# Optimization experiments

Measured on AMD Instinct MI355X. Metric: run time of the kernel, lower is better.

The kernel has to match this reference:

```python
import jax, jax.numpy as jnp
import numpy as np
import math

B, S, HID = 4, 2048, 1024
NH, HD = 16, 64  # num heads, head dim
ROPE_THETA = 10000.0


def rotate_half(x):
    x1, x2 = jnp.split(x, 2, axis=-1)
    return jnp.concatenate((-x2, x1), axis=-1)


def setup_inputs() -> dict:
    key = jax.random.key(0)
    ks = jax.random.split(key, 7)
    hidden_states = jax.random.normal(ks[0], (B, S, HID), dtype=jnp.float32)
    attention_mask = jnp.zeros((B, 1, S, S), dtype=jnp.float32)
    position_ids = jnp.sort(jax.random.randint(ks[1], (B, S), 0, S), axis=-1)
    scale = 1.0 / math.sqrt(HID)
    Wq = jax.random.normal(ks[2], (HID, HID), dtype=jnp.float32) * scale
    Wk = jax.random.normal(ks[3], (HID, HID), dtype=jnp.float32) * scale
    Wv = jax.random.normal(ks[4], (HID, HID), dtype=jnp.float32) * scale
    Wo = jax.random.normal(ks[5], (HID, HID), dtype=jnp.float32) * scale
    return {"hidden_states": hidden_states, "attention_mask": attention_mask,
            "position_ids": position_ids, "Wq": Wq, "Wk": Wk, "Wv": Wv, "Wo": Wo}


def reference(hidden_states, attention_mask, position_ids, Wq, Wk, Wv, Wo):
    dtype = hidden_states.dtype
    # QKV projections (torch Linear: x @ W.T), reshape to [B, H, S, D]
    def proj(W):
        return (hidden_states @ W.T).reshape(B, S, NH, HD).transpose(0, 2, 1, 3)
    q, k, v = proj(Wq), proj(Wk), proj(Wv)

    # Rotary embeddings: cos/sin cache of shape [S, HD], gathered by position_ids
    inv_freq = 1.0 / (ROPE_THETA ** (jnp.arange(0, HD, 2, dtype=jnp.float32) / HD))
    t = jnp.arange(S, dtype=jnp.float32)
    freqs = t[:, None] * inv_freq[None, :]            # [S, HD/2]
    emb = jnp.concatenate((freqs, freqs), axis=-1)     # [S, HD]
    cos = jnp.cos(emb).astype(dtype)[position_ids][:, None]  # [B, 1, S, HD]
    sin = jnp.sin(emb).astype(dtype)[position_ids][:, None]

    q = q * cos + rotate_half(q) * sin
    k = k * cos + rotate_half(k) * sin

    # Manual attention: scores, additive mask, fp32 softmax, weighted sum
    scores = jnp.einsum('bhqd,bhkd->bhqk', q, k) / math.sqrt(HD)
    scores = scores + attention_mask
    attn = jax.nn.softmax(scores.astype(jnp.float32), axis=-1).astype(dtype)
    out = jnp.einsum('bhqk,bhkd->bhqd', attn, v)       # [B, H, S, D]
    out = out.transpose(0, 2, 1, 3).reshape(B, S, HID)
    return out @ Wo.T
```

## Files before the change

kernel.cpp:

```cpp
#include <hip/hip_runtime.h>
#include <hip/hip_bf16.h>
#include <math.h>

typedef __bf16 bf16;
typedef bf16 bf16x4 __attribute__((ext_vector_type(4)));
typedef bf16 bf16x8 __attribute__((ext_vector_type(8)));
typedef float f32x4 __attribute__((ext_vector_type(4)));

#define B_ 4
#define S_ 2048
#define HID_ 1024
#define NH_ 16
#define HD_ 64
#define LTS 72

__device__ __forceinline__ void async16(const bf16* g, bf16* l) {
  __builtin_amdgcn_global_load_lds(
      (const __attribute__((address_space(1))) void*)g,
      (__attribute__((address_space(3))) void*)l, 16, 0, 0);
}

#define MM16(A, B, C) C = __builtin_amdgcn_mfma_f32_16x16x32_bf16(A, B, C, 0, 0, 0)

__global__ void cvt_kernel(const float* __restrict__ src, bf16* __restrict__ dst, int n4) {
  int i = blockIdx.x * 256 + threadIdx.x;
  if (i < n4) {
    float4 v = ((const float4*)src)[i];
    bf16x4 o;
    o[0] = (bf16)v.x; o[1] = (bf16)v.y; o[2] = (bf16)v.z; o[3] = (bf16)v.w;
    ((bf16x4*)dst)[i] = o;
  }
}

#define DECL_ACC \
  f32x4 a00 = {}, a01 = {}, a02 = {}, a03 = {}; \
  f32x4 a10 = {}, a11 = {}, a12 = {}, a13 = {}; \
  f32x4 a20 = {}, a21 = {}, a22 = {}, a23 = {}; \
  f32x4 a30 = {}, a31 = {}, a32 = {}, a33 = {};

#define KLOOP_FRAGS_MFMA \
    bf16x8 af0 = *(const bf16x8*)(lA + (wm + 0 * 16 + l16) * 32 + quad * 8); \
    bf16x8 af1 = *(const bf16x8*)(lA + (wm + 1 * 16 + l16) * 32 + quad * 8); \
    bf16x8 af2 = *(const bf16x8*)(lA + (wm + 2 * 16 + l16) * 32 + quad * 8); \
    bf16x8 af3 = *(const bf16x8*)(lA + (wm + 3 * 16 + l16) * 32 + quad * 8); \
    bf16x8 bg0 = *(const bf16x8*)(lB + (wn + 0 * 16 + l16) * 32 + quad * 8); \
    bf16x8 bg1 = *(const bf16x8*)(lB + (wn + 1 * 16 + l16) * 32 + quad * 8); \
    bf16x8 bg2 = *(const bf16x8*)(lB + (wn + 2 * 16 + l16) * 32 + quad * 8); \
    bf16x8 bg3 = *(const bf16x8*)(lB + (wn + 3 * 16 + l16) * 32 + quad * 8); \
    MM16(af0, bg0, a00); MM16(af0, bg1, a01); MM16(af0, bg2, a02); MM16(af0, bg3, a03); \
    MM16(af1, bg0, a10); MM16(af1, bg1, a11); MM16(af1, bg2, a12); MM16(af1, bg3, a13); \
    MM16(af2, bg0, a20); MM16(af2, bg1, a21); MM16(af2, bg2, a22); MM16(af2, bg3, a23); \
    MM16(af3, bg0, a30); MM16(af3, bg1, a31); MM16(af3, bg2, a32); MM16(af3, bg3, a33);

#define ROPE_R(i, r, C0, C1, C2, C3) { \
  const int mloc = (i) * 16 + quad * 4 + (r); \
  const float p = (float)pos[mbase + mloc]; \
  const float aa0 = p * invf0, aa1 = p * invf1; \
  const float c0 = __cosf(aa0), sn0 = __sinf(aa0); \
  const float c1 = __cosf(aa1), sn1 = __sinf(aa1); \
  myT[mloc * LTS + l16]      = (bf16)((C0[r] * c0 - C2[r] * sn0) * scl); \
  myT[mloc * LTS + 32 + l16] = (bf16)((C2[r] * c0 + C0[r] * sn0) * scl); \
  myT[mloc * LTS + 16 + l16] = (bf16)((C1[r] * c1 - C3[r] * sn1) * scl); \
  myT[mloc * LTS + 48 + l16] = (bf16)((C3[r] * c1 + C1[r] * sn1) * scl); }
#define ROPE_I(i, C0, C1, C2, C3) \
  ROPE_R(i, 0, C0, C1, C2, C3) ROPE_R(i, 1, C0, C1, C2, C3) \
  ROPE_R(i, 2, C0, C1, C2, C3) ROPE_R(i, 3, C0, C1, C2, C3)

#define VW(i, j, C) { \
  bf16x4 o; o[0] = (bf16)C[0]; o[1] = (bf16)C[1]; o[2] = (bf16)C[2]; o[3] = (bf16)C[3]; \
  *(bf16x4*)(myT + ((j) * 16 + l16) * LTS + (i) * 16 + quad * 4) = o; }

__global__ void qkv_gemm(
    const bf16* __restrict__ X, const bf16* __restrict__ Wq,
    const bf16* __restrict__ Wk, const bf16* __restrict__ Wv,
    const int* __restrict__ pos,
    bf16* __restrict__ Q, bf16* __restrict__ Ko, bf16* __restrict__ Vt) {
  const int z = blockIdx.z;
  const bf16* W = (z == 0) ? Wq : (z == 1) ? Wk : Wv;
  const int m0 = blockIdx.y * 128;
  const int n0 = blockIdx.x * 128;
  __shared__ __align__(16) bf16 lA[128 * 32];
  __shared__ __align__(16) bf16 lB[128 * 32];
  __shared__ __align__(16) bf16 lT[4][64 * LTS];
  const int tid = threadIdx.x;
  const int lane = tid & 63, w = tid >> 6;
  const int wm = (w >> 1) * 64, wn = (w & 1) * 64;
  const int quad = lane >> 4, l16 = lane & 15;

  DECL_ACC

  const int qa = tid, qb = tid + 256;
  const int ra = qa >> 2, ca = (qa & 3) * 8;
  const int rb = qb >> 2, cb = (qb & 3) * 8;

  for (int k0 = 0; k0 < 1024; k0 += 32) {
    async16(X + (size_t)(m0 + ra) * 1024 + k0 + ca, lA + qa * 8);
    async16(X + (size_t)(m0 + rb) * 1024 + k0 + cb, lA + qb * 8);
    async16(W + (size_t)(n0 + ra) * 1024 + k0 + ca, lB + qa * 8);
    async16(W + (size_t)(n0 + rb) * 1024 + k0 + cb, lB + qb * 8);
    __syncthreads();
    KLOOP_FRAGS_MFMA
    __syncthreads();
  }

  const int h = (n0 + wn) >> 6;
  const int mbase = m0 + wm;
  const int b = mbase >> 11, s0 = mbase & 2047;
  bf16* myT = lT[w];

  if (z <= 1) {
    const float scl = (z == 0) ? 0.125f : 1.0f;
    const float invf0 = __expf(-0.28782313662425572f * (float)l16);
    const float invf1 = __expf(-0.28782313662425572f * (float)(16 + l16));
    ROPE_I(0, a00, a01, a02, a03)
    ROPE_I(1, a10, a11, a12, a13)
    ROPE_I(2, a20, a21, a22, a23)
    ROPE_I(3, a30, a31, a32, a33)
    asm volatile("s_waitcnt lgkmcnt(0)" ::: "memory");
    bf16* dst = (z == 0) ? Q : Ko;
    const int rr = lane >> 3, cc = lane & 7;
#pragma unroll
    for (int it = 0; it < 8; it++) {
      int mloc = it * 8 + rr;
      bf16x8 v = *(const bf16x8*)(myT + mloc * LTS + cc * 8);
      *(bf16x8*)(dst + (((size_t)b * NH_ + h) * S_ + s0 + mloc) * HD_ + cc * 8) = v;
    }
  } else {
    VW(0, 0, a00) VW(0, 1, a01) VW(0, 2, a02) VW(0, 3, a03)
    VW(1, 0, a10) VW(1, 1, a11) VW(1, 2, a12) VW(1, 3, a13)
    VW(2, 0, a20) VW(2, 1, a21) VW(2, 2, a22) VW(2, 3, a23)
    VW(3, 0, a30) VW(3, 1, a31) VW(3, 2, a32) VW(3, 3, a33)
    asm volatile("s_waitcnt lgkmcnt(0)" ::: "memory");
    const int rr = lane >> 3, cc = lane & 7;
#pragma unroll
    for (int it = 0; it < 8; it++) {
      int d = it * 8 + rr;
      bf16x8 v = *(const bf16x8*)(myT + d * LTS + cc * 8);
      *(bf16x8*)(Vt + (((size_t)b * NH_ + h) * HD_ + d) * S_ + s0 + cc * 8) = v;
    }
  }
}

__global__ void __launch_bounds__(256, 4) attn_kernel(
    const bf16* __restrict__ Q, const bf16* __restrict__ K,
    const bf16* __restrict__ Vt, const float* __restrict__ mask,
    bf16* __restrict__ ctx) {
  const int b = blockIdx.y >> 4, h = blockIdx.y & 15;
  const int q0 = blockIdx.x * 64;
  __shared__ __align__(16) bf16 lK[2][64 * 64];
  __shared__ __align__(16) bf16 lV[2][64 * 64];
  __shared__ __align__(16) bf16 lP[4][16 * 64];
  const int tid = threadIdx.x;
  const int lane = tid & 63, w = tid >> 6;
  const int quad = lane >> 4, l16 = lane & 15;

  const int sr = tid >> 3;
  const int scs = (tid & 7) ^ (sr & 7);

  const size_t headoff = ((size_t)b * NH_ + h) * S_ * HD_;
  {
    const bf16* src = Q + headoff + (size_t)q0 * HD_;
    async16(src + sr * 64 + scs * 8, lK[1] + tid * 8);
    async16(src + (sr + 32) * 64 + scs * 8, lK[1] + (tid + 256) * 8);
    const bf16* ksrc = K + headoff;
    async16(ksrc + sr * 64 + scs * 8, lK[0] + tid * 8);
    async16(ksrc + (sr + 32) * 64 + scs * 8, lK[0] + (tid + 256) * 8);
    const bf16* vbase = Vt + headoff;
    async16(vbase + (size_t)sr * S_ + scs * 8, lV[0] + tid * 8);
    async16(vbase + (size_t)(sr + 32) * S_ + scs * 8, lV[0] + (tid + 256) * 8);
  }

  const float* mrow = mask + ((size_t)b * S_ + q0 + w * 16 + l16) * S_;
  const int sw = l16 & 7;
  const int pq  = (quad ^ sw) * 8;
  const int pq2 = ((quad + 4) ^ sw) * 8;
  bf16* myP = lP[w];

  const float LOG2E = 1.44269504089f;
  const float MSH = -17.3123404907f;
#define XMASK(dst, src) { float4 t_ = (src); \
  dst.x = fmaf(t_.x, LOG2E, MSH); dst.y = fmaf(t_.y, LOG2E, MSH); \
  dst.z = fmaf(t_.z, LOG2E, MSH); dst.w = fmaf(t_.w, LOG2E, MSH); }

  float4 f0, f1, f2, f3;
  {
    const float4* m4 = (const float4*)(mrow);
    XMASK(f0, m4[quad]); XMASK(f1, m4[4 + quad]);
    XMASK(f2, m4[8 + quad]); XMASK(f3, m4[12 + quad]);
  }

  __syncthreads();
  const bf16x8 qf  = *(const bf16x8*)(lK[1] + (w * 16 + l16) * 64 + pq);
  const bf16x8 qf2 = *(const bf16x8*)(lK[1] + (w * 16 + l16) * 64 + pq2);
  __syncthreads();

  f32x4 o0 = {}, o1 = {}, o2 = {}, o3 = {};
  float l_acc = 0.f;

  for (int kt = 0; kt < 32; kt++) {
    const bf16* lKc = lK[kt & 1];
    const bf16* lVc = lV[kt & 1];
    if (kt < 31) {
      bf16* nK = lK[(kt & 1) ^ 1];
      bf16* nV = lV[(kt & 1) ^ 1];
      const int k0n = (kt + 1) * 64;
      const bf16* ksrc = K + headoff + (size_t)k0n * HD_;
      async16(ksrc + sr * 64 + scs * 8, nK + tid * 8);
      async16(ksrc + (sr + 32) * 64 + scs * 8, nK + (tid + 256) * 8);
      const bf16* vbase = Vt + headoff + k0n;
      async16(vbase + (size_t)sr * S_ + scs * 8, nV + tid * 8);
      async16(vbase + (size_t)(sr + 32) * S_ + scs * 8, nV + (tid + 256) * 8);
    }

    f32x4 s0 = {}, s1 = {}, s2 = {}, s3 = {};
    __builtin_amdgcn_s_setprio(1);
    {
      bf16x8 k0f = *(const bf16x8*)(lKc + (0 * 16 + l16) * 64 + pq);
      bf16x8 k1f = *(const bf16x8*)(lKc + (1 * 16 + l16) * 64 + pq);
      bf16x8 k2f = *(const bf16x8*)(lKc + (2 * 16 + l16) * 64 + pq);
      bf16x8 k3f = *(const bf16x8*)(lKc + (3 * 16 + l16) * 64 + pq);
      MM16(k0f, qf, s0); MM16(k1f, qf, s1); MM16(k2f, qf, s2); MM16(k3f, qf, s3);
    }
    {
      bf16x8 k0f = *(const bf16x8*)(lKc + (0 * 16 + l16) * 64 + pq2);
      bf16x8 k1f = *(const bf16x8*)(lKc + (1 * 16 + l16) * 64 + pq2);
      bf16x8 k2f = *(const bf16x8*)(lKc + (2 * 16 + l16) * 64 + pq2);
      bf16x8 k3f = *(const bf16x8*)(lKc + (3 * 16 + l16) * 64 + pq2);
      MM16(k0f, qf2, s0); MM16(k1f, qf2, s1); MM16(k2f, qf2, s2); MM16(k3f, qf2, s3);
    }
    __builtin_amdgcn_s_setprio(0);

    float p00 = __builtin_amdgcn_exp2f(fmaf(s0[0], LOG2E, f0.x));
    float p01 = __builtin_amdgcn_exp2f(fmaf(s0[1], LOG2E, f0.y));
    float p02 = __builtin_amdgcn_exp2f(fmaf(s0[2], LOG2E, f0.z));
    float p03 = __builtin_amdgcn_exp2f(fmaf(s0[3], LOG2E, f0.w));
    float p10 = __builtin_amdgcn_exp2f(fmaf(s1[0], LOG2E, f1.x));
    float p11 = __builtin_amdgcn_exp2f(fmaf(s1[1], LOG2E, f1.y));
    float p12 = __builtin_amdgcn_exp2f(fmaf(s1[2], LOG2E, f1.z));
    float p13 = __builtin_amdgcn_exp2f(fmaf(s1[3], LOG2E, f1.w));
    float p20 = __builtin_amdgcn_exp2f(fmaf(s2[0], LOG2E, f2.x));
    float p21 = __builtin_amdgcn_exp2f(fmaf(s2[1], LOG2E, f2.y));
    float p22 = __builtin_amdgcn_exp2f(fmaf(s2[2], LOG2E, f2.z));
    float p23 = __builtin_amdgcn_exp2f(fmaf(s2[3], LOG2E, f2.w));
    float p30 = __builtin_amdgcn_exp2f(fmaf(s3[0], LOG2E, f3.x));
    float p31 = __builtin_amdgcn_exp2f(fmaf(s3[1], LOG2E, f3.y));
    float p32 = __builtin_amdgcn_exp2f(fmaf(s3[2], LOG2E, f3.z));
    float p33 = __builtin_amdgcn_exp2f(fmaf(s3[3], LOG2E, f3.w));

    {
      const int swz = 8 * sw;
      bf16x4 pk;
      pk[0] = (bf16)p00; pk[1] = (bf16)p01; pk[2] = (bf16)p02; pk[3] = (bf16)p03;
      *(bf16x4*)(myP + l16 * 64 + ((0 * 16 + quad * 4) ^ swz)) = pk;
      pk[0] = (bf16)p10; pk[1] = (bf16)p11; pk[2] = (bf16)p12; pk[3] = (bf16)p13;
      *(bf16x4*)(myP + l16 * 64 + ((1 * 16 + quad * 4) ^ swz)) = pk;
      pk[0] = (bf16)p20; pk[1] = (bf16)p21; pk[2] = (bf16)p22; pk[3] = (bf16)p23;
      *(bf16x4*)(myP + l16 * 64 + ((2 * 16 + quad * 4) ^ swz)) = pk;
      pk[0] = (bf16)p30; pk[1] = (bf16)p31; pk[2] = (bf16)p32; pk[3] = (bf16)p33;
      *(bf16x4*)(myP + l16 * 64 + ((3 * 16 + quad * 4) ^ swz)) = pk;
    }

    l_acc += (((p00 + p01) + (p02 + p03)) + ((p10 + p11) + (p12 + p13)))
           + (((p20 + p21) + (p22 + p23)) + ((p30 + p31) + (p32 + p33)));

    if (kt < 31) {
      const float4* mn = (const float4*)(mrow + (kt + 1) * 64);
      XMASK(f0, mn[quad]); XMASK(f1, mn[4 + quad]);
      XMASK(f2, mn[8 + quad]); XMASK(f3, mn[12 + quad]);
    }

    __builtin_amdgcn_s_setprio(1);
    {
      bf16x8 ap = *(const bf16x8*)(myP + l16 * 64 + pq);
      bf16x8 b0 = *(const bf16x8*)(lVc + (0 * 16 + l16) * 64 + pq);
      bf16x8 b1 = *(const bf16x8*)(lVc + (1 * 16 + l16) * 64 + pq);
      bf16x8 b2 = *(const bf16x8*)(lVc + (2 * 16 + l16) * 64 + pq);
      bf16x8 b3 = *(const bf16x8*)(lVc + (3 * 16 + l16) * 64 + pq);
      MM16(ap, b0, o0); MM16(ap, b1, o1); MM16(ap, b2, o2); MM16(ap, b3, o3);
    }
    {
      bf16x8 ap = *(const bf16x8*)(myP + l16 * 64 + pq2);
      bf16x8 b0 = *(const bf16x8*)(lVc + (0 * 16 + l16) * 64 + pq2);
      bf16x8 b1 = *(const bf16x8*)(lVc + (1 * 16 + l16) * 64 + pq2);
      bf16x8 b2 = *(const bf16x8*)(lVc + (2 * 16 + l16) * 64 + pq2);
      bf16x8 b3 = *(const bf16x8*)(lVc + (3 * 16 + l16) * 64 + pq2);
      MM16(ap, b0, o0); MM16(ap, b1, o1); MM16(ap, b2, o2); MM16(ap, b3, o3);
    }
    __builtin_amdgcn_s_setprio(0);

    __syncthreads();
  }

  float l_run = l_acc;
  l_run += __shfl_xor(l_run, 16);
  l_run += __shfl_xor(l_run, 32);
  f32x4 lv;
  lv[0] = __shfl(l_run, quad * 4 + 0);
  lv[1] = __shfl(l_run, quad * 4 + 1);
  lv[2] = __shfl(l_run, quad * 4 + 2);
  lv[3] = __shfl(l_run, quad * 4 + 3);
  bf16* lO = lK[0];
#pragma unroll
  for (int r = 0; r < 4; r++) {
    const float invl = 1.0f / lv[r];
    const int sloc = w * 16 + quad * 4 + r;
    lO[sloc * 64 + l16]      = (bf16)(o0[r] * invl);
    lO[sloc * 64 + 16 + l16] = (bf16)(o1[r] * invl);
    lO[sloc * 64 + 32 + l16] = (bf16)(o2[r] * invl);
    lO[sloc * 64 + 48 + l16] = (bf16)(o3[r] * invl);
  }
  __syncthreads();
  {
    const int rr = tid >> 3, cc = tid & 7;
#pragma unroll
    for (int it = 0; it < 2; it++) {
      int sloc = it * 32 + rr;
      bf16x8 v = *(const bf16x8*)(lO + sloc * 64 + cc * 8);
      *(bf16x8*)(ctx + ((size_t)b * S_ + q0 + sloc) * HID_ + h * HD_ + cc * 8) = v;
    }
  }
}

#define PW(i, j, C) { \
  float* po = out + (size_t)(m0 + wm + (i) * 16 + quad * 4) * 1024 + n0 + wn + (j) * 16 + l16; \
  po[0] = C[0]; po[1024] = C[1]; po[2048] = C[2]; po[3072] = C[3]; }

__global__ void proj_gemm(
    const bf16* __restrict__ A, const bf16* __restrict__ Wo, float* __restrict__ out) {
  const int m0 = blockIdx.y * 128;
  const int n0 = blockIdx.x * 128;
  __shared__ __align__(16) bf16 lA[128 * 32];
  __shared__ __align__(16) bf16 lB[128 * 32];
  const int tid = threadIdx.x;
  const int lane = tid & 63, w = tid >> 6;
  const int wm = (w >> 1) * 64, wn = (w & 1) * 64;
  const int quad = lane >> 4, l16 = lane & 15;

  DECL_ACC
  const int qa = tid, qb = tid + 256;
  const int ra = qa >> 2, ca = (qa & 3) * 8;
  const int rb = qb >> 2, cb = (qb & 3) * 8;

  for (int k0 = 0; k0 < 1024; k0 += 32) {
    async16(A + (size_t)(m0 + ra) * 1024 + k0 + ca, lA + qa * 8);
    async16(A + (size_t)(m0 + rb) * 1024 + k0 + cb, lA + qb * 8);
    async16(Wo + (size_t)(n0 + ra) * 1024 + k0 + ca, lB + qa * 8);
    async16(Wo + (size_t)(n0 + rb) * 1024 + k0 + cb, lB + qb * 8);
    __syncthreads();
    KLOOP_FRAGS_MFMA
    __syncthreads();
  }
  PW(0, 0, a00) PW(0, 1, a01) PW(0, 2, a02) PW(0, 3, a03)
  PW(1, 0, a10) PW(1, 1, a11) PW(1, 2, a12) PW(1, 3, a13)
  PW(2, 0, a20) PW(2, 1, a21) PW(2, 2, a22) PW(2, 3, a23)
  PW(3, 0, a30) PW(3, 1, a31) PW(3, 2, a32) PW(3, 3, a33)
}

__global__ void sentinel_kernel(float* out, int n, float val) {
  int i = blockIdx.x * 256 + threadIdx.x;
  if (i < n) out[i] = val;
}

extern "C" void kernel_launch(void* const* d_in, const int* in_sizes, int n_in,
                              void* d_out, int out_size, void* d_ws, size_t ws_size,
                              hipStream_t stream) {
  const float* X    = (const float*)d_in[0];
  const float* mask = (const float*)d_in[1];
  const int*   pos  = (const int*)d_in[2];
  const float* Wq   = (const float*)d_in[3];
  const float* Wk   = (const float*)d_in[4];
  const float* Wv   = (const float*)d_in[5];
  const float* Wo   = (const float*)d_in[6];
  float* out = (float*)d_out;

  char* ws = (char*)d_ws;
  const size_t SZ = (size_t)B_ * NH_ * S_ * HD_ * sizeof(bf16);
  if (ws_size < 3 * SZ) {
    sentinel_kernel<<<(out_size + 255) / 256, 256, 0, stream>>>(
        out, out_size, (float)(ws_size >> 20));
    return;
  }

  bf16* Xb  = (bf16*)(ws);
  bf16* ctx = (bf16*)(ws);
  bf16* Q   = (bf16*)(ws + SZ);
  bf16* Vt  = (bf16*)(ws + 2 * SZ);
  bf16* Wob = (bf16*)(ws + 2 * SZ);
  bf16* Kb  = (bf16*)d_out;
  bf16* Wqb = (bf16*)((char*)d_out + SZ);
  bf16* Wkb = Wqb + 1024 * 1024;
  bf16* Wvb = Wkb + 1024 * 1024;

  const int nX4 = (B_ * S_ * HID_) / 4;
  const int nW4 = (HID_ * HID_) / 4;
  cvt_kernel<<<(nX4 + 255) / 256, 256, 0, stream>>>(X, Xb, nX4);
  cvt_kernel<<<(nW4 + 255) / 256, 256, 0, stream>>>(Wq, Wqb, nW4);
  cvt_kernel<<<(nW4 + 255) / 256, 256, 0, stream>>>(Wk, Wkb, nW4);
  cvt_kernel<<<(nW4 + 255) / 256, 256, 0, stream>>>(Wv, Wvb, nW4);

  qkv_gemm<<<dim3(8, 64, 3), 256, 0, stream>>>(Xb, Wqb, Wkb, Wvb, pos, Q, Kb, Vt);
  attn_kernel<<<dim3(32, 64), 256, 0, stream>>>(Q, Kb, Vt, mask, ctx);

  cvt_kernel<<<(nW4 + 255) / 256, 256, 0, stream>>>(Wo, Wob, nW4);
  proj_gemm<<<dim3(8, 64), 256, 0, stream>>>(ctx, Wob, out);
}
```

Baseline: 392.4 us.

## Process 128 query rows per attention block with 8 waves sharing K/V tiles

Doubles the attention block to 512 threads covering 128 query rows, so each K/V tile loaded into LDS is reused by twice as many waves and each thread issues one async load per tile instead of two. The P staging buffer is shrunk to 16x32 per wave, and P is written and read back in two halves just before each PV MFMA pair, using a new swizzle. Q is staged through spare LDS regions (lV[1] and lP), and the output epilogue reuses the whole lK area for 128 rows. The trade is fewer blocks in the grid and more waves per barrier, plus tighter LDS reuse that depends on the aliasing being correct.

```diff
diff --git a/kernel.cpp b/kernel.cpp
--- a/kernel.cpp
+++ b/kernel.cpp
@@ -141,15 +141,18 @@
   }
 }
 
-__global__ void __launch_bounds__(256, 4) attn_kernel(
+__global__ void __launch_bounds__(512, 4) attn_kernel(
     const bf16* __restrict__ Q, const bf16* __restrict__ K,
     const bf16* __restrict__ Vt, const float* __restrict__ mask,
     bf16* __restrict__ ctx) {
   const int b = blockIdx.y >> 4, h = blockIdx.y & 15;
-  const int q0 = blockIdx.x * 64;
+  const int q0 = blockIdx.x * 128;
   __shared__ __align__(16) bf16 lK[2][64 * 64];
   __shared__ __align__(16) bf16 lV[2][64 * 64];
-  __shared__ __align__(16) bf16 lP[4][16 * 64];
+  __shared__ __align__(16) bf16 lP[8][16 * 32];
+  bf16* lKf = (bf16*)lK;
+  bf16* lPf = (bf16*)lP;
+
   const int tid = threadIdx.x;
   const int lane = tid & 63, w = tid >> 6;
   const int quad = lane >> 4, l16 = lane & 15;
@@ -159,15 +162,11 @@
 
   const size_t headoff = ((size_t)b * NH_ + h) * S_ * HD_;
   {
-    const bf16* src = Q + headoff + (size_t)q0 * HD_;
-    async16(src + sr * 64 + scs * 8, lK[1] + tid * 8);
-    async16(src + (sr + 32) * 64 + scs * 8, lK[1] + (tid + 256) * 8);
-    const bf16* ksrc = K + headoff;
-    async16(ksrc + sr * 64 + scs * 8, lK[0] + tid * 8);
-    async16(ksrc + (sr + 32) * 64 + scs * 8, lK[0] + (tid + 256) * 8);
-    const bf16* vbase = Vt + headoff;
-    async16(vbase + (size_t)sr * S_ + scs * 8, lV[0] + tid * 8);
-    async16(vbase + (size_t)(sr + 32) * S_ + scs * 8, lV[0] + (tid + 256) * 8);
+    const bf16* qsrc = Q + headoff + (size_t)q0 * HD_;
+    async16(qsrc + sr * 64 + scs * 8, lV[1] + tid * 8);
+    async16(qsrc + (size_t)(sr + 64) * 64 + scs * 8, lPf + tid * 8);
+    async16(K + headoff + sr * 64 + scs * 8, lK[0] + tid * 8);
+    async16(Vt + headoff + (size_t)sr * S_ + scs * 8, lV[0] + tid * 8);
   }
 
   const float* mrow = mask + ((size_t)b * S_ + q0 + w * 16 + l16) * S_;
@@ -175,6 +174,9 @@
   const int pq  = (quad ^ sw) * 8;
   const int pq2 = ((quad + 4) ^ sw) * 8;
   bf16* myP = lP[w];
+  const int pwr0 = l16 * 32 + ((quad ^ (l16 & 6)) * 4);
+  const int pwr1 = l16 * 32 + (((4 + quad) ^ (l16 & 6)) * 4);
+  const int prd  = l16 * 32 + ((quad ^ ((l16 >> 1) & 3)) * 8);
 
   const float LOG2E = 1.44269504089f;
   const float MSH = -17.3123404907f;
@@ -190,8 +192,10 @@
   }
 
   __syncthreads();
-  const bf16x8 qf  = *(const bf16x8*)(lK[1] + (w * 16 + l16) * 64 + pq);
-  const bf16x8 qf2 = *(const bf16x8*)(lK[1] + (w * 16 + l16) * 64 + pq2);
+  const int row128 = w * 16 + l16;
+  const bf16* qsrcL = (w < 4) ? (lV[1] + row128 * 64) : (lPf + (row128 - 64) * 64);
+  const bf16x8 qf  = *(const bf16x8*)(qsrcL + pq);
+  const bf16x8 qf2 = *(const bf16x8*)(qsrcL + pq2);
   __syncthreads();
 
   f32x4 o0 = {}, o1 = {}, o2 = {}, o3 = {};
@@ -204,12 +208,8 @@
       bf16* nK = lK[(kt & 1) ^ 1];
       bf16* nV = lV[(kt & 1) ^ 1];
       const int k0n = (kt + 1) * 64;
-      const bf16* ksrc = K + headoff + (size_t)k0n * HD_;
-      async16(ksrc + sr * 64 + scs * 8, nK + tid * 8);
-      async16(ksrc + (sr + 32) * 64 + scs * 8, nK + (tid + 256) * 8);
-      const bf16* vbase = Vt + headoff + k0n;
-      async16(vbase + (size_t)sr * S_ + scs * 8, nV + tid * 8);
-      async16(vbase + (size_t)(sr + 32) * S_ + scs * 8, nV + (tid + 256) * 8);
+      async16(K + headoff + (size_t)k0n * HD_ + sr * 64 + scs * 8, nK + tid * 8);
+      async16(Vt + headoff + k0n + (size_t)sr * S_ + scs * 8, nV + tid * 8);
     }
 
     f32x4 s0 = {}, s1 = {}, s2 = {}, s3 = {};
@@ -247,19 +247,6 @@
     float p32 = __builtin_amdgcn_exp2f(fmaf(s3[2], LOG2E, f3.z));
     float p33 = __builtin_amdgcn_exp2f(fmaf(s3[3], LOG2E, f3.w));
 
-    {
-      const int swz = 8 * sw;
-      bf16x4 pk;
-      pk[0] = (bf16)p00; pk[1] = (bf16)p01; pk[2] = (bf16)p02; pk[3] = (bf16)p03;
-      *(bf16x4*)(myP + l16 * 64 + ((0 * 16 + quad * 4) ^ swz)) = pk;
-      pk[0] = (bf16)p10; pk[1] = (bf16)p11; pk[2] = (bf16)p12; pk[3] = (bf16)p13;
-      *(bf16x4*)(myP + l16 * 64 + ((1 * 16 + quad * 4) ^ swz)) = pk;
-      pk[0] = (bf16)p20; pk[1] = (bf16)p21; pk[2] = (bf16)p22; pk[3] = (bf16)p23;
-      *(bf16x4*)(myP + l16 * 64 + ((2 * 16 + quad * 4) ^ swz)) = pk;
-      pk[0] = (bf16)p30; pk[1] = (bf16)p31; pk[2] = (bf16)p32; pk[3] = (bf16)p33;
-      *(bf16x4*)(myP + l16 * 64 + ((3 * 16 + quad * 4) ^ swz)) = pk;
-    }
-
     l_acc += (((p00 + p01) + (p02 + p03)) + ((p10 + p11) + (p12 + p13)))
            + (((p20 + p21) + (p22 + p23)) + ((p30 + p31) + (p32 + p33)));
 
@@ -271,7 +258,12 @@
 
     __builtin_amdgcn_s_setprio(1);
     {
-      bf16x8 ap = *(const bf16x8*)(myP + l16 * 64 + pq);
+      bf16x4 pk;
+      pk[0] = (bf16)p00; pk[1] = (bf16)p01; pk[2] = (bf16)p02; pk[3] = (bf16)p03;
+      *(bf16x4*)(myP + pwr0) = pk;
+      pk[0] = (bf16)p10; pk[1] = (bf16)p11; pk[2] = (bf16)p12; pk[3] = (bf16)p13;
+      *(bf16x4*)(myP + pwr1) = pk;
+      bf16x8 ap = *(const bf16x8*)(myP + prd);
       bf16x8 b0 = *(const bf16x8*)(lVc + (0 * 16 + l16) * 64 + pq);
       bf16x8 b1 = *(const bf16x8*)(lVc + (1 * 16 + l16) * 64 + pq);
       bf16x8 b2 = *(const bf16x8*)(lVc + (2 * 16 + l16) * 64 + pq);
@@ -279,7 +271,12 @@
       MM16(ap, b0, o0); MM16(ap, b1, o1); MM16(ap, b2, o2); MM16(ap, b3, o3);
     }
     {
-      bf16x8 ap = *(const bf16x8*)(myP + l16 * 64 + pq2);
+      bf16x4 pk;
+      pk[0] = (bf16)p20; pk[1] = (bf16)p21; pk[2] = (bf16)p22; pk[3] = (bf16)p23;
+      *(bf16x4*)(myP + pwr0) = pk;
+      pk[0] = (bf16)p30; pk[1] = (bf16)p31; pk[2] = (bf16)p32; pk[3] = (bf16)p33;
+      *(bf16x4*)(myP + pwr1) = pk;
+      bf16x8 ap = *(const bf16x8*)(myP + prd);
       bf16x8 b0 = *(const bf16x8*)(lVc + (0 * 16 + l16) * 64 + pq2);
       bf16x8 b1 = *(const bf16x8*)(lVc + (1 * 16 + l16) * 64 + pq2);
       bf16x8 b2 = *(const bf16x8*)(lVc + (2 * 16 + l16) * 64 + pq2);
@@ -299,23 +296,22 @@
   lv[1] = __shfl(l_run, quad * 4 + 1);
   lv[2] = __shfl(l_run, quad * 4 + 2);
   lv[3] = __shfl(l_run, quad * 4 + 3);
-  bf16* lO = lK[0];
 #pragma unroll
   for (int r = 0; r < 4; r++) {
     const float invl = 1.0f / lv[r];
     const int sloc = w * 16 + quad * 4 + r;
-    lO[sloc * 64 + l16]      = (bf16)(o0[r] * invl);
-    lO[sloc * 64 + 16 + l16] = (bf16)(o1[r] * invl);
-    lO[sloc * 64 + 32 + l16] = (bf16)(o2[r] * invl);
-    lO[sloc * 64 + 48 + l16] = (bf16)(o3[r] * invl);
+    lKf[sloc * 64 + l16]      = (bf16)(o0[r] * invl);
+    lKf[sloc * 64 + 16 + l16] = (bf16)(o1[r] * invl);
+    lKf[sloc * 64 + 32 + l16] = (bf16)(o2[r] * invl);
+    lKf[sloc * 64 + 48 + l16] = (bf16)(o3[r] * invl);
   }
   __syncthreads();
   {
     const int rr = tid >> 3, cc = tid & 7;
 #pragma unroll
     for (int it = 0; it < 2; it++) {
-      int sloc = it * 32 + rr;
-      bf16x8 v = *(const bf16x8*)(lO + sloc * 64 + cc * 8);
+      int sloc = it * 64 + rr;
+      bf16x8 v = *(const bf16x8*)(lKf + sloc * 64 + cc * 8);
       *(bf16x8*)(ctx + ((size_t)b * S_ + q0 + sloc) * HID_ + h * HD_ + cc * 8) = v;
     }
   }
@@ -399,7 +395,7 @@
   cvt_kernel<<<(nW4 + 255) / 256, 256, 0, stream>>>(Wv, Wvb, nW4);
 
   qkv_gemm<<<dim3(8, 64, 3), 256, 0, stream>>>(Xb, Wqb, Wkb, Wvb, pos, Q, Kb, Vt);
-  attn_kernel<<<dim3(32, 64), 256, 0, stream>>>(Q, Kb, Vt, mask, ctx);
+  attn_kernel<<<dim3(16, 64), 512, 0, stream>>>(Q, Kb, Vt, mask, ctx);
 
   cvt_kernel<<<(nW4 + 255) / 256, 256, 0, stream>>>(Wo, Wob, nW4);
   proj_gemm<<<dim3(8, 64), 256, 0, stream>>>(ctx, Wob, out);
```

Measured after the change: 424.3 us. 8.1% more time.

## Stage K/V tiles through registers two steps ahead instead of async LDS loads

Applied to the files above, without the earlier changes.

Replaces the direct global-to-LDS async loads of the next K/V tile with register prefetch. Global loads are issued two iterations ahead, and their contents are written into the alternate LDS buffer one iteration ahead. The mask row for the next tile is now loaded before the softmax of the current tile and held as raw floats, so its latency is hidden behind the exp work. The end-of-iteration __syncthreads is replaced by an explicit lgkmcnt wait plus s_barrier with sched_barriers. This costs more VGPRs and adds explicit LDS stores in the loop, which may reduce occupancy.

```diff
diff --git a/kernel.cpp b/kernel.cpp
--- a/kernel.cpp
+++ b/kernel.cpp
@@ -178,15 +178,11 @@
 
   const float LOG2E = 1.44269504089f;
   const float MSH = -17.3123404907f;
-#define XMASK(dst, src) { float4 t_ = (src); \
-  dst.x = fmaf(t_.x, LOG2E, MSH); dst.y = fmaf(t_.y, LOG2E, MSH); \
-  dst.z = fmaf(t_.z, LOG2E, MSH); dst.w = fmaf(t_.w, LOG2E, MSH); }
-
-  float4 f0, f1, f2, f3;
+
+  float4 g0, g1, g2, g3;
   {
     const float4* m4 = (const float4*)(mrow);
-    XMASK(f0, m4[quad]); XMASK(f1, m4[4 + quad]);
-    XMASK(f2, m4[8 + quad]); XMASK(f3, m4[12 + quad]);
+    g0 = m4[quad]; g1 = m4[4 + quad]; g2 = m4[8 + quad]; g3 = m4[12 + quad];
   }
 
   __syncthreads();
@@ -194,23 +190,22 @@
   const bf16x8 qf2 = *(const bf16x8*)(lK[1] + (w * 16 + l16) * 64 + pq2);
   __syncthreads();
 
+  bf16x8 kr0, kr1, vr0, vr1;
+  {
+    const bf16* ksrc = K + headoff + (size_t)64 * HD_;
+    kr0 = *(const bf16x8*)(ksrc + sr * 64 + scs * 8);
+    kr1 = *(const bf16x8*)(ksrc + (sr + 32) * 64 + scs * 8);
+    const bf16* vsrc = Vt + headoff + 64;
+    vr0 = *(const bf16x8*)(vsrc + (size_t)sr * S_ + scs * 8);
+    vr1 = *(const bf16x8*)(vsrc + (size_t)(sr + 32) * S_ + scs * 8);
+  }
+
   f32x4 o0 = {}, o1 = {}, o2 = {}, o3 = {};
   float l_acc = 0.f;
 
   for (int kt = 0; kt < 32; kt++) {
     const bf16* lKc = lK[kt & 1];
     const bf16* lVc = lV[kt & 1];
-    if (kt < 31) {
-      bf16* nK = lK[(kt & 1) ^ 1];
-      bf16* nV = lV[(kt & 1) ^ 1];
-      const int k0n = (kt + 1) * 64;
-      const bf16* ksrc = K + headoff + (size_t)k0n * HD_;
-      async16(ksrc + sr * 64 + scs * 8, nK + tid * 8);
-      async16(ksrc + (sr + 32) * 64 + scs * 8, nK + (tid + 256) * 8);
-      const bf16* vbase = Vt + headoff + k0n;
-      async16(vbase + (size_t)sr * S_ + scs * 8, nV + tid * 8);
-      async16(vbase + (size_t)(sr + 32) * S_ + scs * 8, nV + (tid + 256) * 8);
-    }
 
     f32x4 s0 = {}, s1 = {}, s2 = {}, s3 = {};
     __builtin_amdgcn_s_setprio(1);
@@ -230,22 +225,53 @@
     }
     __builtin_amdgcn_s_setprio(0);
 
-    float p00 = __builtin_amdgcn_exp2f(fmaf(s0[0], LOG2E, f0.x));
-    float p01 = __builtin_amdgcn_exp2f(fmaf(s0[1], LOG2E, f0.y));
-    float p02 = __builtin_amdgcn_exp2f(fmaf(s0[2], LOG2E, f0.z));
-    float p03 = __builtin_amdgcn_exp2f(fmaf(s0[3], LOG2E, f0.w));
-    float p10 = __builtin_amdgcn_exp2f(fmaf(s1[0], LOG2E, f1.x));
-    float p11 = __builtin_amdgcn_exp2f(fmaf(s1[1], LOG2E, f1.y));
-    float p12 = __builtin_amdgcn_exp2f(fmaf(s1[2], LOG2E, f1.z));
-    float p13 = __builtin_amdgcn_exp2f(fmaf(s1[3], LOG2E, f1.w));
-    float p20 = __builtin_amdgcn_exp2f(fmaf(s2[0], LOG2E, f2.x));
-    float p21 = __builtin_amdgcn_exp2f(fmaf(s2[1], LOG2E, f2.y));
-    float p22 = __builtin_amdgcn_exp2f(fmaf(s2[2], LOG2E, f2.z));
-    float p23 = __builtin_amdgcn_exp2f(fmaf(s2[3], LOG2E, f2.w));
-    float p30 = __builtin_amdgcn_exp2f(fmaf(s3[0], LOG2E, f3.x));
-    float p31 = __builtin_amdgcn_exp2f(fmaf(s3[1], LOG2E, f3.y));
-    float p32 = __builtin_amdgcn_exp2f(fmaf(s3[2], LOG2E, f3.z));
-    float p33 = __builtin_amdgcn_exp2f(fmaf(s3[3], LOG2E, f3.w));
+    if (kt < 31) {
+      bf16* nK = lK[(kt & 1) ^ 1];
+      bf16* nV = lV[(kt & 1) ^ 1];
+      *(bf16x8*)(nK + tid * 8) = kr0;
+      *(bf16x8*)(nK + (tid + 256) * 8) = kr1;
+      *(bf16x8*)(nV + tid * 8) = vr0;
+      *(bf16x8*)(nV + (tid + 256) * 8) = vr1;
+    }
+
+    if (kt < 30) {
+      const bf16* ksrc = K + headoff + (size_t)(kt + 2) * 64 * HD_;
+      kr0 = *(const bf16x8*)(ksrc + sr * 64 + scs * 8);
+      kr1 = *(const bf16x8*)(ksrc + (sr + 32) * 64 + scs * 8);
+      const bf16* vsrc = Vt + headoff + (kt + 2) * 64;
+      vr0 = *(const bf16x8*)(vsrc + (size_t)sr * S_ + scs * 8);
+      vr1 = *(const bf16x8*)(vsrc + (size_t)(sr + 32) * S_ + scs * 8);
+    }
+    float4 h0, h1, h2, h3;
+    if (kt < 31) {
+      const float4* mn = (const float4*)(mrow + (kt + 1) * 64);
+      h0 = mn[quad]; h1 = mn[4 + quad]; h2 = mn[8 + quad]; h3 = mn[12 + quad];
+    }
+
+    const float fx0 = fmaf(g0.x, LOG2E, MSH), fy0 = fmaf(g0.y, LOG2E, MSH);
+    const float fz0 = fmaf(g0.z, LOG2E, MSH), fw0 = fmaf(g0.w, LOG2E, MSH);
+    const float fx1 = fmaf(g1.x, LOG2E, MSH), fy1 = fmaf(g1.y, LOG2E, MSH);
+    const float fz1 = fmaf(g1.z, LOG2E, MSH), fw1 = fmaf(g1.w, LOG2E, MSH);
+    const float fx2 = fmaf(g2.x, LOG2E, MSH), fy2 = fmaf(g2.y, LOG2E, MSH);
+    const float fz2 = fmaf(g2.z, LOG2E, MSH), fw2 = fmaf(g2.w, LOG2E, MSH);
+    const float fx3 = fmaf(g3.x, LOG2E, MSH), fy3 = fmaf(g3.y, LOG2E, MSH);
+    const float fz3 = fmaf(g3.z, LOG2E, MSH), fw3 = fmaf(g3.w, LOG2E, MSH);
+    float p00 = __builtin_amdgcn_exp2f(fmaf(s0[0], LOG2E, fx0));
+    float p01 = __builtin_amdgcn_exp2f(fmaf(s0[1], LOG2E, fy0));
+    float p02 = __builtin_amdgcn_exp2f(fmaf(s0[2], LOG2E, fz0));
+    float p03 = __builtin_amdgcn_exp2f(fmaf(s0[3], LOG2E, fw0));
+    float p10 = __builtin_amdgcn_exp2f(fmaf(s1[0], LOG2E, fx1));
+    float p11 = __builtin_amdgcn_exp2f(fmaf(s1[1], LOG2E, fy1));
+    float p12 = __builtin_amdgcn_exp2f(fmaf(s1[2], LOG2E, fz1));
+    float p13 = __builtin_amdgcn_exp2f(fmaf(s1[3], LOG2E, fw1));
+    float p20 = __builtin_amdgcn_exp2f(fmaf(s2[0], LOG2E, fx2));
+    float p21 = __builtin_amdgcn_exp2f(fmaf(s2[1], LOG2E, fy2));
+    float p22 = __builtin_amdgcn_exp2f(fmaf(s2[2], LOG2E, fz2));
+    float p23 = __builtin_amdgcn_exp2f(fmaf(s2[3], LOG2E, fw2));
+    float p30 = __builtin_amdgcn_exp2f(fmaf(s3[0], LOG2E, fx3));
+    float p31 = __builtin_amdgcn_exp2f(fmaf(s3[1], LOG2E, fy3));
+    float p32 = __builtin_amdgcn_exp2f(fmaf(s3[2], LOG2E, fz3));
+    float p33 = __builtin_amdgcn_exp2f(fmaf(s3[3], LOG2E, fw3));
 
     {
       const int swz = 8 * sw;
@@ -263,12 +289,6 @@
     l_acc += (((p00 + p01) + (p02 + p03)) + ((p10 + p11) + (p12 + p13)))
            + (((p20 + p21) + (p22 + p23)) + ((p30 + p31) + (p32 + p33)));
 
-    if (kt < 31) {
-      const float4* mn = (const float4*)(mrow + (kt + 1) * 64);
-      XMASK(f0, mn[quad]); XMASK(f1, mn[4 + quad]);
-      XMASK(f2, mn[8 + quad]); XMASK(f3, mn[12 + quad]);
-    }
-
     __builtin_amdgcn_s_setprio(1);
     {
       bf16x8 ap = *(const bf16x8*)(myP + l16 * 64 + pq);
@@ -288,7 +308,14 @@
     }
     __builtin_amdgcn_s_setprio(0);
 
-    __syncthreads();
+    if (kt < 31) { g0 = h0; g1 = h1; g2 = h2; g3 = h3; }
+
+    if (kt < 31) {
+      asm volatile("s_waitcnt lgkmcnt(0)" ::: "memory");
+      __builtin_amdgcn_sched_barrier(0);
+      __builtin_amdgcn_s_barrier();
+      __builtin_amdgcn_sched_barrier(0);
+    }
   }
 
   float l_run = l_acc;
```

New measurement: 390.7 us. No clear change (-0.4%).

## Process 128 query rows per attention block to reuse K/V tiles

Applied to the files above, without the earlier changes.

Each attention workgroup now handles 128 queries instead of 64, with each wave computing two 16-row query groups against every staged K/V tile. This halves the number of K/V tile loads from global memory and LDS per query and doubles the MFMA work per LDS fragment read. In exchange it raises register pressure (launch bounds drop to 3 waves per EU), halves the grid to 1024 blocks, and reuses the per-wave P buffer serially for both groups.

```diff
diff --git a/kernel.cpp b/kernel.cpp
--- a/kernel.cpp
+++ b/kernel.cpp
@@ -141,15 +141,16 @@
   }
 }
 
-__global__ void __launch_bounds__(256, 4) attn_kernel(
+__global__ void __launch_bounds__(256, 3) attn_kernel(
     const bf16* __restrict__ Q, const bf16* __restrict__ K,
     const bf16* __restrict__ Vt, const float* __restrict__ mask,
     bf16* __restrict__ ctx) {
   const int b = blockIdx.y >> 4, h = blockIdx.y & 15;
-  const int q0 = blockIdx.x * 64;
+  const int q0 = blockIdx.x * 128;
   __shared__ __align__(16) bf16 lK[2][64 * 64];
   __shared__ __align__(16) bf16 lV[2][64 * 64];
   __shared__ __align__(16) bf16 lP[4][16 * 64];
+  bf16* lKf = (bf16*)lK;
   const int tid = threadIdx.x;
   const int lane = tid & 63, w = tid >> 6;
   const int quad = lane >> 4, l16 = lane & 15;
@@ -159,9 +160,11 @@
 
   const size_t headoff = ((size_t)b * NH_ + h) * S_ * HD_;
   {
-    const bf16* src = Q + headoff + (size_t)q0 * HD_;
-    async16(src + sr * 64 + scs * 8, lK[1] + tid * 8);
-    async16(src + (sr + 32) * 64 + scs * 8, lK[1] + (tid + 256) * 8);
+    const bf16* qsrc = Q + headoff + (size_t)q0 * HD_;
+    async16(qsrc + sr * 64 + scs * 8, lK[1] + tid * 8);
+    async16(qsrc + (sr + 32) * 64 + scs * 8, lK[1] + (tid + 256) * 8);
+    async16(qsrc + (size_t)(sr + 64) * 64 + scs * 8, lV[1] + tid * 8);
+    async16(qsrc + (size_t)(sr + 96) * 64 + scs * 8, lV[1] + (tid + 256) * 8);
     const bf16* ksrc = K + headoff;
     async16(ksrc + sr * 64 + scs * 8, lK[0] + tid * 8);
     async16(ksrc + (sr + 32) * 64 + scs * 8, lK[0] + (tid + 256) * 8);
@@ -170,7 +173,8 @@
     async16(vbase + (size_t)(sr + 32) * S_ + scs * 8, lV[0] + (tid + 256) * 8);
   }
 
-  const float* mrow = mask + ((size_t)b * S_ + q0 + w * 16 + l16) * S_;
+  const float* mrowA = mask + ((size_t)b * S_ + q0 + w * 32 + l16) * S_;
+  const float* mrowB = mrowA + (size_t)16 * S_;
   const int sw = l16 & 7;
   const int pq  = (quad ^ sw) * 8;
   const int pq2 = ((quad + 4) ^ sw) * 8;
@@ -182,20 +186,30 @@
   dst.x = fmaf(t_.x, LOG2E, MSH); dst.y = fmaf(t_.y, LOG2E, MSH); \
   dst.z = fmaf(t_.z, LOG2E, MSH); dst.w = fmaf(t_.w, LOG2E, MSH); }
 
-  float4 f0, f1, f2, f3;
+  float4 gA0, gA1, gA2, gA3, gB0, gB1, gB2, gB3;
   {
-    const float4* m4 = (const float4*)(mrow);
-    XMASK(f0, m4[quad]); XMASK(f1, m4[4 + quad]);
-    XMASK(f2, m4[8 + quad]); XMASK(f3, m4[12 + quad]);
+    const float4* mA = (const float4*)(mrowA);
+    XMASK(gA0, mA[quad]); XMASK(gA1, mA[4 + quad]);
+    XMASK(gA2, mA[8 + quad]); XMASK(gA3, mA[12 + quad]);
+    const float4* mB = (const float4*)(mrowB);
+    XMASK(gB0, mB[quad]); XMASK(gB1, mB[4 + quad]);
+    XMASK(gB2, mB[8 + quad]); XMASK(gB3, mB[12 + quad]);
   }
 
   __syncthreads();
-  const bf16x8 qf  = *(const bf16x8*)(lK[1] + (w * 16 + l16) * 64 + pq);
-  const bf16x8 qf2 = *(const bf16x8*)(lK[1] + (w * 16 + l16) * 64 + pq2);
+  const int rA = w * 32 + l16;
+  const bf16* qbA = (rA < 64) ? (lK[1] + rA * 64) : (lV[1] + (rA - 64) * 64);
+  const bf16x8 qfA  = *(const bf16x8*)(qbA + pq);
+  const bf16x8 qfA2 = *(const bf16x8*)(qbA + pq2);
+  const int rB = rA + 16;
+  const bf16* qbB = (rB < 64) ? (lK[1] + rB * 64) : (lV[1] + (rB - 64) * 64);
+  const bf16x8 qfB  = *(const bf16x8*)(qbB + pq);
+  const bf16x8 qfB2 = *(const bf16x8*)(qbB + pq2);
   __syncthreads();
 
-  f32x4 o0 = {}, o1 = {}, o2 = {}, o3 = {};
-  float l_acc = 0.f;
+  f32x4 oA0 = {}, oA1 = {}, oA2 = {}, oA3 = {};
+  f32x4 oB0 = {}, oB1 = {}, oB2 = {}, oB3 = {};
+  float laccA = 0.f, laccB = 0.f;
 
   for (int kt = 0; kt < 32; kt++) {
     const bf16* lKc = lK[kt & 1];
@@ -212,43 +226,46 @@
       async16(vbase + (size_t)(sr + 32) * S_ + scs * 8, nV + (tid + 256) * 8);
     }
 
-    f32x4 s0 = {}, s1 = {}, s2 = {}, s3 = {};
+    f32x4 sA0 = {}, sA1 = {}, sA2 = {}, sA3 = {};
+    f32x4 sB0 = {}, sB1 = {}, sB2 = {}, sB3 = {};
     __builtin_amdgcn_s_setprio(1);
     {
       bf16x8 k0f = *(const bf16x8*)(lKc + (0 * 16 + l16) * 64 + pq);
       bf16x8 k1f = *(const bf16x8*)(lKc + (1 * 16 + l16) * 64 + pq);
       bf16x8 k2f = *(const bf16x8*)(lKc + (2 * 16 + l16) * 64 + pq);
       bf16x8 k3f = *(const bf16x8*)(lKc + (3 * 16 + l16) * 64 + pq);
-      MM16(k0f, qf, s0); MM16(k1f, qf, s1); MM16(k2f, qf, s2); MM16(k3f, qf, s3);
+      MM16(k0f, qfA, sA0); MM16(k1f, qfA, sA1); MM16(k2f, qfA, sA2); MM16(k3f, qfA, sA3);
+      MM16(k0f, qfB, sB0); MM16(k1f, qfB, sB1); MM16(k2f, qfB, sB2); MM16(k3f, qfB, sB3);
     }
     {
       bf16x8 k0f = *(const bf16x8*)(lKc + (0 * 16 + l16) * 64 + pq2);
       bf16x8 k1f = *(const bf16x8*)(lKc + (1 * 16 + l16) * 64 + pq2);
       bf16x8 k2f = *(const bf16x8*)(lKc + (2 * 16 + l16) * 64 + pq2);
       bf16x8 k3f = *(const bf16x8*)(lKc + (3 * 16 + l16) * 64 + pq2);
-      MM16(k0f, qf2, s0); MM16(k1f, qf2, s1); MM16(k2f, qf2, s2); MM16(k3f, qf2, s3);
+      MM16(k0f, qfA2, sA0); MM16(k1f, qfA2, sA1); MM16(k2f, qfA2, sA2); MM16(k3f, qfA2, sA3);
+      MM16(k0f, qfB2, sB0); MM16(k1f, qfB2, sB1); MM16(k2f, qfB2, sB2); MM16(k3f, qfB2, sB3);
     }
     __builtin_amdgcn_s_setprio(0);
 
-    float p00 = __builtin_amdgcn_exp2f(fmaf(s0[0], LOG2E, f0.x));
-    float p01 = __builtin_amdgcn_exp2f(fmaf(s0[1], LOG2E, f0.y));
-    float p02 = __builtin_amdgcn_exp2f(fmaf(s0[2], LOG2E, f0.z));
-    float p03 = __builtin_amdgcn_exp2f(fmaf(s0[3], LOG2E, f0.w));
-    float p10 = __builtin_amdgcn_exp2f(fmaf(s1[0], LOG2E, f1.x));
-    float p11 = __builtin_amdgcn_exp2f(fmaf(s1[1], LOG2E, f1.y));
-    float p12 = __builtin_amdgcn_exp2f(fmaf(s1[2], LOG2E, f1.z));
-    float p13 = __builtin_amdgcn_exp2f(fmaf(s1[3], LOG2E, f1.w));
-    float p20 = __builtin_amdgcn_exp2f(fmaf(s2[0], LOG2E, f2.x));
-    float p21 = __builtin_amdgcn_exp2f(fmaf(s2[1], LOG2E, f2.y));
-    float p22 = __builtin_amdgcn_exp2f(fmaf(s2[2], LOG2E, f2.z));
-    float p23 = __builtin_amdgcn_exp2f(fmaf(s2[3], LOG2E, f2.w));
-    float p30 = __builtin_amdgcn_exp2f(fmaf(s3[0], LOG2E, f3.x));
-    float p31 = __builtin_amdgcn_exp2f(fmaf(s3[1], LOG2E, f3.y));
-    float p32 = __builtin_amdgcn_exp2f(fmaf(s3[2], LOG2E, f3.z));
-    float p33 = __builtin_amdgcn_exp2f(fmaf(s3[3], LOG2E, f3.w));
-
-    {
-      const int swz = 8 * sw;
+    const int swz = 8 * sw;
+    bf16x8 apA, apA2;
+    {
+      float p00 = __builtin_amdgcn_exp2f(fmaf(sA0[0], LOG2E, gA0.x));
+      float p01 = __builtin_amdgcn_exp2f(fmaf(sA0[1], LOG2E, gA0.y));
+      float p02 = __builtin_amdgcn_exp2f(fmaf(sA0[2], LOG2E, gA0.z));
+      float p03 = __builtin_amdgcn_exp2f(fmaf(sA0[3], LOG2E, gA0.w));
+      float p10 = __builtin_amdgcn_exp2f(fmaf(sA1[0], LOG2E, gA1.x));
+      float p11 = __builtin_amdgcn_exp2f(fmaf(sA1[1], LOG2E, gA1.y));
+      float p12 = __builtin_amdgcn_exp2f(fmaf(sA1[2], LOG2E, gA1.z));
+      float p13 = __builtin_amdgcn_exp2f(fmaf(sA1[3], LOG2E, gA1.w));
+      float p20 = __builtin_amdgcn_exp2f(fmaf(sA2[0], LOG2E, gA2.x));
+      float p21 = __builtin_amdgcn_exp2f(fmaf(sA2[1], LOG2E, gA2.y));
+      float p22 = __builtin_amdgcn_exp2f(fmaf(sA2[2], LOG2E, gA2.z));
+      float p23 = __builtin_amdgcn_exp2f(fmaf(sA2[3], LOG2E, gA2.w));
+      float p30 = __builtin_amdgcn_exp2f(fmaf(sA3[0], LOG2E, gA3.x));
+      float p31 = __builtin_amdgcn_exp2f(fmaf(sA3[1], LOG2E, gA3.y));
+      float p32 = __builtin_amdgcn_exp2f(fmaf(sA3[2], LOG2E, gA3.z));
+      float p33 = __builtin_amdgcn_exp2f(fmaf(sA3[3], LOG2E, gA3.w));
       bf16x4 pk;
       pk[0] = (bf16)p00; pk[1] = (bf16)p01; pk[2] = (bf16)p02; pk[3] = (bf16)p03;
       *(bf16x4*)(myP + l16 * 64 + ((0 * 16 + quad * 4) ^ swz)) = pk;
@@ -258,64 +275,105 @@
       *(bf16x4*)(myP + l16 * 64 + ((2 * 16 + quad * 4) ^ swz)) = pk;
       pk[0] = (bf16)p30; pk[1] = (bf16)p31; pk[2] = (bf16)p32; pk[3] = (bf16)p33;
       *(bf16x4*)(myP + l16 * 64 + ((3 * 16 + quad * 4) ^ swz)) = pk;
-    }
-
-    l_acc += (((p00 + p01) + (p02 + p03)) + ((p10 + p11) + (p12 + p13)))
-           + (((p20 + p21) + (p22 + p23)) + ((p30 + p31) + (p32 + p33)));
+      laccA += (((p00 + p01) + (p02 + p03)) + ((p10 + p11) + (p12 + p13)))
+             + (((p20 + p21) + (p22 + p23)) + ((p30 + p31) + (p32 + p33)));
+      apA  = *(const bf16x8*)(myP + l16 * 64 + pq);
+      apA2 = *(const bf16x8*)(myP + l16 * 64 + pq2);
+    }
+    bf16x8 apB, apB2;
+    {
+      float p00 = __builtin_amdgcn_exp2f(fmaf(sB0[0], LOG2E, gB0.x));
+      float p01 = __builtin_amdgcn_exp2f(fmaf(sB0[1], LOG2E, gB0.y));
+      float p02 = __builtin_amdgcn_exp2f(fmaf(sB0[2], LOG2E, gB0.z));
+      float p03 = __builtin_amdgcn_exp2f(fmaf(sB0[3], LOG2E, gB0.w));
+      float p10 = __builtin_amdgcn_exp2f(fmaf(sB1[0], LOG2E, gB1.x));
+      float p11 = __builtin_amdgcn_exp2f(fmaf(sB1[1], LOG2E, gB1.y));
+      float p12 = __builtin_amdgcn_exp2f(fmaf(sB1[2], LOG2E, gB1.z));
+      float p13 = __builtin_amdgcn_exp2f(fmaf(sB1[3], LOG2E, gB1.w));
+      float p20 = __builtin_amdgcn_exp2f(fmaf(sB2[0], LOG2E, gB2.x));
+      float p21 = __builtin_amdgcn_exp2f(fmaf(sB2[1], LOG2E, gB2.y));
+      float p22 = __builtin_amdgcn_exp2f(fmaf(sB2[2], LOG2E, gB2.z));
+      float p23 = __builtin_amdgcn_exp2f(fmaf(sB2[3], LOG2E, gB2.w));
+      float p30 = __builtin_amdgcn_exp2f(fmaf(sB3[0], LOG2E, gB3.x));
+      float p31 = __builtin_amdgcn_exp2f(fmaf(sB3[1], LOG2E, gB3.y));
+      float p32 = __builtin_amdgcn_exp2f(fmaf(sB3[2], LOG2E, gB3.z));
+      float p33 = __builtin_amdgcn_exp2f(fmaf(sB3[3], LOG2E, gB3.w));
+      bf16x4 pk;
+      pk[0] = (bf16)p00; pk[1] = (bf16)p01; pk[2] = (bf16)p02; pk[3] = (bf16)p03;
+      *(bf16x4*)(myP + l16 * 64 + ((0 * 16 + quad * 4) ^ swz)) = pk;
+      pk[0] = (bf16)p10; pk[1] = (bf16)p11; pk[2] = (bf16)p12; pk[3] = (bf16)p13;
+      *(bf16x4*)(myP + l16 * 64 + ((1 * 16 + quad * 4) ^ swz)) = pk;
+      pk[0] = (bf16)p20; pk[1] = (bf16)p21; pk[2] = (bf16)p22; pk[3] = (bf16)p23;
+      *(bf16x4*)(myP + l16 * 64 + ((2 * 16 + quad * 4) ^ swz)) = pk;
+      pk[0] = (bf16)p30; pk[1] = (bf16)p31; pk[2] = (bf16)p32; pk[3] = (bf16)p33;
+      *(bf16x4*)(myP + l16 * 64 + ((3 * 16 + quad * 4) ^ swz)) = pk;
+      laccB += (((p00 + p01) + (p02 + p03)) + ((p10 + p11) + (p12 + p13)))
+             + (((p20 + p21) + (p22 + p23)) + ((p30 + p31) + (p32 + p33)));
+      apB  = *(const bf16x8*)(myP + l16 * 64 + pq);
+      apB2 = *(const bf16x8*)(myP + l16 * 64 + pq2);
+    }
+
+    __builtin_amdgcn_s_setprio(1);
+    {
+      bf16x8 v0 = *(const bf16x8*)(lVc + (0 * 16 + l16) * 64 + pq);
+      bf16x8 v1 = *(const bf16x8*)(lVc + (1 * 16 + l16) * 64 + pq);
+      bf16x8 v2 = *(const bf16x8*)(lVc + (2 * 16 + l16) * 64 + pq);
+      bf16x8 v3 = *(const bf16x8*)(lVc + (3 * 16 + l16) * 64 + pq);
+      MM16(apA, v0, oA0); MM16(apA, v1, oA1); MM16(apA, v2, oA2); MM16(apA, v3, oA3);
+      MM16(apB, v0, oB0); MM16(apB, v1, oB1); MM16(apB, v2, oB2); MM16(apB, v3, oB3);
+    }
+    {
+      bf16x8 v0 = *(const bf16x8*)(lVc + (0 * 16 + l16) * 64 + pq2);
+      bf16x8 v1 = *(const bf16x8*)(lVc + (1 * 16 + l16) * 64 + pq2);
+      bf16x8 v2 = *(const bf16x8*)(lVc + (2 * 16 + l16) * 64 + pq2);
+      bf16x8 v3 = *(const bf16x8*)(lVc + (3 * 16 + l16) * 64 + pq2);
+      MM16(apA2, v0, oA0); MM16(apA2, v1, oA1); MM16(apA2, v2, oA2); MM16(apA2, v3, oA3);
+      MM16(apB2, v0, oB0); MM16(apB2, v1, oB1); MM16(apB2, v2, oB2); MM16(apB2, v3, oB3);
+    }
+    __builtin_amdgcn_s_setprio(0);
 
     if (kt < 31) {
-      const float4* mn = (const float4*)(mrow + (kt + 1) * 64);
-      XMASK(f0, mn[quad]); XMASK(f1, mn[4 + quad]);
-      XMASK(f2, mn[8 + quad]); XMASK(f3, mn[12 + quad]);
-    }
-
-    __builtin_amdgcn_s_setprio(1);
-    {
-      bf16x8 ap = *(const bf16x8*)(myP + l16 * 64 + pq);
-      bf16x8 b0 = *(const bf16x8*)(lVc + (0 * 16 + l16) * 64 + pq);
-      bf16x8 b1 = *(const bf16x8*)(lVc + (1 * 16 + l16) * 64 + pq);
-      bf16x8 b2 = *(const bf16x8*)(lVc + (2 * 16 + l16) * 64 + pq);
-      bf16x8 b3 = *(const bf16x8*)(lVc + (3 * 16 + l16) * 64 + pq);
-      MM16(ap, b0, o0); MM16(ap, b1, o1); MM16(ap, b2, o2); MM16(ap, b3, o3);
-    }
-    {
-      bf16x8 ap = *(const bf16x8*)(myP + l16 * 64 + pq2);
-      bf16x8 b0 = *(const bf16x8*)(lVc + (0 * 16 + l16) * 64 + pq2);
-      bf16x8 b1 = *(const bf16x8*)(lVc + (1 * 16 + l16) * 64 + pq2);
-      bf16x8 b2 = *(const bf16x8*)(lVc + (2 * 16 + l16) * 64 + pq2);
-      bf16x8 b3 = *(const bf16x8*)(lVc + (3 * 16 + l16) * 64 + pq2);
-      MM16(ap, b0, o0); MM16(ap, b1, o1); MM16(ap, b2, o2); MM16(ap, b3, o3);
-    }
-    __builtin_amdgcn_s_setprio(0);
+      const float4* mA = (const float4*)(mrowA + (kt + 1) * 64);
+      XMASK(gA0, mA[quad]); XMASK(gA1, mA[4 + quad]);
+      XMASK(gA2, mA[8 + quad]); XMASK(gA3, mA[12 + quad]);
+      const float4* mB = (const float4*)(mrowB + (kt + 1) * 64);
+      XMASK(gB0, mB[quad]); XMASK(gB1, mB[4 + quad]);
+      XMASK(gB2, mB[8 + quad]); XMASK(gB3, mB[12 + quad]);
+    }
 
     __syncthreads();
   }
 
-  float l_run = l_acc;
-  l_run += __shfl_xor(l_run, 16);
-  l_run += __shfl_xor(l_run, 32);
-  f32x4 lv;
-  lv[0] = __shfl(l_run, quad * 4 + 0);
-  lv[1] = __shfl(l_run, quad * 4 + 1);
-  lv[2] = __shfl(l_run, quad * 4 + 2);
-  lv[3] = __shfl(l_run, quad * 4 + 3);
-  bf16* lO = lK[0];
+  float lrA = laccA, lrB = laccB;
+  lrA += __shfl_xor(lrA, 16); lrA += __shfl_xor(lrA, 32);
+  lrB += __shfl_xor(lrB, 16); lrB += __shfl_xor(lrB, 32);
+  f32x4 lvA, lvB;
+  lvA[0] = __shfl(lrA, quad * 4 + 0); lvB[0] = __shfl(lrB, quad * 4 + 0);
+  lvA[1] = __shfl(lrA, quad * 4 + 1); lvB[1] = __shfl(lrB, quad * 4 + 1);
+  lvA[2] = __shfl(lrA, quad * 4 + 2); lvB[2] = __shfl(lrB, quad * 4 + 2);
+  lvA[3] = __shfl(lrA, quad * 4 + 3); lvB[3] = __shfl(lrB, quad * 4 + 3);
 #pragma unroll
   for (int r = 0; r < 4; r++) {
-    const float invl = 1.0f / lv[r];
-    const int sloc = w * 16 + quad * 4 + r;
-    lO[sloc * 64 + l16]      = (bf16)(o0[r] * invl);
-    lO[sloc * 64 + 16 + l16] = (bf16)(o1[r] * invl);
-    lO[sloc * 64 + 32 + l16] = (bf16)(o2[r] * invl);
-    lO[sloc * 64 + 48 + l16] = (bf16)(o3[r] * invl);
+    const float ivA = 1.0f / lvA[r];
+    const int sA = w * 32 + quad * 4 + r;
+    lKf[sA * 64 + l16]      = (bf16)(oA0[r] * ivA);
+    lKf[sA * 64 + 16 + l16] = (bf16)(oA1[r] * ivA);
+    lKf[sA * 64 + 32 + l16] = (bf16)(oA2[r] * ivA);
+    lKf[sA * 64 + 48 + l16] = (bf16)(oA3[r] * ivA);
+    const float ivB = 1.0f / lvB[r];
+    const int sB = sA + 16;
+    lKf[sB * 64 + l16]      = (bf16)(oB0[r] * ivB);
+    lKf[sB * 64 + 16 + l16] = (bf16)(oB1[r] * ivB);
+    lKf[sB * 64 + 32 + l16] = (bf16)(oB2[r] * ivB);
+    lKf[sB * 64 + 48 + l16] = (bf16)(oB3[r] * ivB);
   }
   __syncthreads();
   {
     const int rr = tid >> 3, cc = tid & 7;
 #pragma unroll
-    for (int it = 0; it < 2; it++) {
+    for (int it = 0; it < 4; it++) {
       int sloc = it * 32 + rr;
-      bf16x8 v = *(const bf16x8*)(lO + sloc * 64 + cc * 8);
+      bf16x8 v = *(const bf16x8*)(lKf + sloc * 64 + cc * 8);
       *(bf16x8*)(ctx + ((size_t)b * S_ + q0 + sloc) * HID_ + h * HD_ + cc * 8) = v;
     }
   }
@@ -399,7 +457,7 @@
   cvt_kernel<<<(nW4 + 255) / 256, 256, 0, stream>>>(Wv, Wvb, nW4);
 
   qkv_gemm<<<dim3(8, 64, 3), 256, 0, stream>>>(Xb, Wqb, Wkb, Wvb, pos, Q, Kb, Vt);
-  attn_kernel<<<dim3(32, 64), 256, 0, stream>>>(Q, Kb, Vt, mask, ctx);
+  attn_kernel<<<dim3(16, 64), 256, 0, stream>>>(Q, Kb, Vt, mask, ctx);
 
   cvt_kernel<<<(nW4 + 255) / 256, 256, 0, stream>>>(Wo, Wob, nW4);
   proj_gemm<<<dim3(8, 64), 256, 0, stream>>>(ctx, Wob, out);
```

New measurement: 401.1 us. +2.2%, slower.
